# Optimization experiments

Measured on AMD Instinct MI355X. Metric: run time of the kernel, lower is better.

The kernel has to match this reference:

```python
import jax, jax.numpy as jnp
import numpy as np

# alpha clamp limits: balance=False -> [exp(-1/5), exp(-1/25)]
ALPHA_MIN = float(np.exp(-1.0 / 5.0))
ALPHA_MAX = float(np.exp(-1.0 / 25.0))
T_CROP = 100


def setup_inputs() -> dict:
    key = jax.random.key(0)
    k1, k2, k3 = jax.random.split(key, 3)
    B, T, D, H = 128, 1000, 1024, 256
    x = jax.random.normal(k1, (B, T, D), dtype=jnp.float32)
    bound = float(np.sqrt(1.0 / D))
    W = jax.random.uniform(k2, (H, D), minval=-bound, maxval=bound, dtype=jnp.float32)
    alpha = jax.random.uniform(k3, (H,), minval=ALPHA_MIN, maxval=ALPHA_MAX, dtype=jnp.float32)
    return {"x": x, "W": W, "alpha": alpha}


def reference(x, W, alpha):
    # x: [B, T, D], W: [H, D], alpha: [H]
    a = jnp.clip(alpha, ALPHA_MIN, ALPHA_MAX)
    Wx = jnp.einsum('btd,hd->bth', x, W)  # [B, T, H]
    T = Wx.shape[1]
    mask = (jnp.arange(T) >= T_CROP).astype(Wx.dtype)  # [T]
    Wx_t = jnp.moveaxis(Wx, 1, 0)  # [T, B, H]

    def step(carry, inp):
        ut, out = carry
        wx, m = inp
        ut = a * ut + (1.0 - a) * wx
        out = out + m * jax.nn.softmax(ut, axis=-1)
        return (ut, out), None

    B, H = Wx.shape[0], Wx.shape[2]
    init = (jnp.zeros((B, H), Wx.dtype), jnp.zeros((B, H), Wx.dtype))
    (_, out), _ = jax.lax.scan(step, init, (Wx_t, mask))
    return out  # [B, H]
```

## Files before the change

kernel.cpp:

```cpp
#include <hip/hip_runtime.h>
#include <hip/hip_bf16.h>

#define B_    128
#define T_    1000
#define D_    1024
#define H_    256
#define TCROP 100
#define CHUNK 20
#define NCH   50
#define CSKIP 5

typedef __attribute__((ext_vector_type(8))) short bfrag8;
typedef __attribute__((ext_vector_type(4))) float f32x4;
typedef unsigned long long ull;

__device__ __forceinline__ unsigned short f2bf(float f) {
    union { float f; unsigned int u; } v; v.f = f;
    unsigned int u = v.u;
    u += 0x7FFFu + ((u >> 16) & 1u);
    return (unsigned short)(u >> 16);
}
__device__ __forceinline__ float bf2f(unsigned short u) {
    union { unsigned int u; float f; } v; v.u = ((unsigned int)u) << 16;
    return v.f;
}
__device__ __forceinline__ bfrag8 cvt8(float4 f0, float4 f1) {
    bfrag8 v;
    v[0] = (short)f2bf(f0.x); v[1] = (short)f2bf(f0.y);
    v[2] = (short)f2bf(f0.z); v[3] = (short)f2bf(f0.w);
    v[4] = (short)f2bf(f1.x); v[5] = (short)f2bf(f1.y);
    v[6] = (short)f2bf(f1.z); v[7] = (short)f2bf(f1.w);
    return v;
}

__global__ __launch_bounds__(256) void wconv_kernel(
        const float* __restrict__ W, unsigned short* __restrict__ Wbf) {
    const int i = (blockIdx.x * 256 + threadIdx.x) * 8;
    float4 f0 = *(const float4*)(W + i);
    float4 f1 = *(const float4*)(W + i + 4);
    *(bfrag8*)(Wbf + i) = cvt8(f0, f1);
}

__global__ __launch_bounds__(512) void gemm_kernel(
        const float* __restrict__ x, const unsigned short* __restrict__ Wbf,
        unsigned short* __restrict__ Wx) {
    __shared__ unsigned short As[2][128 * 64];
    __shared__ unsigned short Bs[2][256 * 64];

    const int tid  = threadIdx.x;
    const int lane = tid & 63;
    const int wave = tid >> 6;
    const int wr   = wave >> 2;
    const int wc   = wave & 3;
    const int m0   = blockIdx.x * 128;

    f32x4 acc[4][4];
#pragma unroll
    for (int m = 0; m < 4; ++m)
#pragma unroll
        for (int n = 0; n < 4; ++n) acc[m][n] = (f32x4){0.f, 0.f, 0.f, 0.f};

    const int rr  = lane & 15;
    const int kh  = lane >> 4;
    const int ra0 = tid >> 3;
    const int ja  = tid & 7;
    const int sa  = (ja ^ (ra0 & 7)) * 8;
    const float* ap0 = x + (size_t)(m0 + ra0) * D_ + ja * 8;
    const float* ap1 = ap0 + (size_t)64 * D_;

#pragma unroll
    for (int q = 0; q < 4; ++q) {
        const int li = q * 512 + tid;
        const int r = li >> 3, j = li & 7;
        const int jj = j ^ (r & 7);
        __builtin_amdgcn_global_load_lds(
            (const __attribute__((address_space(1))) void*)(Wbf + (size_t)r * D_ + jj * 8),
            (__attribute__((address_space(3))) void*)&Bs[0][li * 8], 16, 0, 0);
    }
    {
        float4 f00 = *(const float4*)ap0;
        float4 f01 = *(const float4*)(ap0 + 4);
        float4 f10 = *(const float4*)ap1;
        float4 f11 = *(const float4*)(ap1 + 4);
        *(bfrag8*)&As[0][ra0 * 64 + sa]        = cvt8(f00, f01);
        *(bfrag8*)&As[0][(ra0 + 64) * 64 + sa] = cvt8(f10, f11);
    }
    asm volatile("s_waitcnt vmcnt(0) lgkmcnt(0)" ::: "memory");
    __builtin_amdgcn_sched_barrier(0);
    __builtin_amdgcn_s_barrier();

    for (int it = 0; it < 16; ++it) {
        const int cur = it & 1, nxt = cur ^ 1;
        float4 f00, f01, f10, f11;
        if (it < 15) {
            const int ktn = (it + 1) * 64;
            f00 = *(const float4*)(ap0 + ktn);
            f01 = *(const float4*)(ap0 + ktn + 4);
            f10 = *(const float4*)(ap1 + ktn);
            f11 = *(const float4*)(ap1 + ktn + 4);
#pragma unroll
            for (int q = 0; q < 4; ++q) {
                const int li = q * 512 + tid;
                const int r = li >> 3, j = li & 7;
                const int jj = j ^ (r & 7);
                __builtin_amdgcn_global_load_lds(
                    (const __attribute__((address_space(1))) void*)
                        (Wbf + (size_t)r * D_ + ktn + jj * 8),
                    (__attribute__((address_space(3))) void*)&Bs[nxt][li * 8], 16, 0, 0);
            }
        }
        __builtin_amdgcn_sched_barrier(0);
#pragma unroll
        for (int kk = 0; kk < 2; ++kk) {
            const int c16 = kk * 4 + kh;
            bfrag8 af[4], bfr[4];
#pragma unroll
            for (int m = 0; m < 4; ++m) {
                const int row = wr * 64 + m * 16 + rr;
                af[m] = *(const bfrag8*)&As[cur][row * 64 + ((c16 ^ (row & 7)) * 8)];
            }
#pragma unroll
            for (int n = 0; n < 4; ++n) {
                const int row = wc * 64 + n * 16 + rr;
                bfr[n] = *(const bfrag8*)&Bs[cur][row * 64 + ((c16 ^ (row & 7)) * 8)];
            }
#pragma unroll
            for (int m = 0; m < 4; ++m)
#pragma unroll
                for (int n = 0; n < 4; ++n)
                    acc[m][n] = __builtin_amdgcn_mfma_f32_16x16x32_bf16(
                        af[m], bfr[n], acc[m][n], 0, 0, 0);
        }
        if (it < 15) {
            *(bfrag8*)&As[nxt][ra0 * 64 + sa]        = cvt8(f00, f01);
            *(bfrag8*)&As[nxt][(ra0 + 64) * 64 + sa] = cvt8(f10, f11);
        }
        asm volatile("s_waitcnt vmcnt(0) lgkmcnt(0)" ::: "memory");
        __builtin_amdgcn_sched_barrier(0);
        __builtin_amdgcn_s_barrier();
    }

    const int cl = lane & 15, rg = lane >> 4;
#pragma unroll
    for (int m = 0; m < 4; ++m)
#pragma unroll
        for (int n = 0; n < 4; ++n)
#pragma unroll
            for (int j = 0; j < 4; ++j) {
                const int row = m0 + wr * 64 + m * 16 + rg * 4 + j;
                const int col = wc * 64 + n * 16 + cl;
                Wx[(size_t)row * H_ + col] = f2bf(acc[m][n][j]);
            }
}

__global__ __launch_bounds__(64) void scanA_kernel(
        const unsigned short* __restrict__ Wx, const float* __restrict__ alpha,
        float* __restrict__ F) {
    const int c = blockIdx.x, b = blockIdx.y;
    const int lane = threadIdx.x;
    const int h = lane * 4;

    const float AMIN = 0.81873075307798182f, AMAX = 0.96078943915232320f;
    float4 al = *(const float4*)(alpha + h);
    float a[4]  = {fminf(fmaxf(al.x, AMIN), AMAX), fminf(fmaxf(al.y, AMIN), AMAX),
                   fminf(fmaxf(al.z, AMIN), AMAX), fminf(fmaxf(al.w, AMIN), AMAX)};
    float om[4] = {1.f - a[0], 1.f - a[1], 1.f - a[2], 1.f - a[3]};

    float ut[4] = {0.f, 0.f, 0.f, 0.f};
    const unsigned short* base = Wx + ((size_t)b * T_ + c * CHUNK) * H_ + h;
#pragma unroll 4
    for (int t = 0; t < CHUNK; ++t) {
        ull wv = *(const ull*)(base + (size_t)t * H_);
        ut[0] = a[0] * ut[0] + om[0] * bf2f((unsigned short)wv);
        ut[1] = a[1] * ut[1] + om[1] * bf2f((unsigned short)(wv >> 16));
        ut[2] = a[2] * ut[2] + om[2] * bf2f((unsigned short)(wv >> 32));
        ut[3] = a[3] * ut[3] + om[3] * bf2f((unsigned short)(wv >> 48));
    }
    float4 o; o.x = ut[0]; o.y = ut[1]; o.z = ut[2]; o.w = ut[3];
    *(float4*)(F + ((size_t)b * NCH + c) * H_ + h) = o;
}

__global__ __launch_bounds__(256) void scanB_kernel(
        const float* __restrict__ F, const float* __restrict__ alpha,
        float* __restrict__ S) {
    const int b = blockIdx.x, h = threadIdx.x;
    const float AMIN = 0.81873075307798182f, AMAX = 0.96078943915232320f;
    const float a = fminf(fmaxf(alpha[h], AMIN), AMAX);
    const float aL = powf(a, (float)CHUNK);
    float s = 0.f;
    for (int c = 0; c < NCH; ++c) {
        S[((size_t)b * NCH + c) * H_ + h] = s;
        s = aL * s + F[((size_t)b * NCH + c) * H_ + h];
    }
}

__global__ __launch_bounds__(64) void scanC_kernel(
        const unsigned short* __restrict__ Wx, const float* __restrict__ alpha,
        const float* __restrict__ S, float* __restrict__ P) {
    const int c = blockIdx.x + CSKIP;
    const int b = blockIdx.y;
    const int lane = threadIdx.x;
    const int h = lane * 4;

    const float AMIN = 0.81873075307798182f, AMAX = 0.96078943915232320f;
    float4 al = *(const float4*)(alpha + h);
    float a[4]  = {fminf(fmaxf(al.x, AMIN), AMAX), fminf(fmaxf(al.y, AMIN), AMAX),
                   fminf(fmaxf(al.z, AMIN), AMAX), fminf(fmaxf(al.w, AMIN), AMAX)};
    float om[4] = {1.f - a[0], 1.f - a[1], 1.f - a[2], 1.f - a[3]};

    float4 s0 = *(const float4*)(S + ((size_t)b * NCH + c) * H_ + h);
    float ut[4]   = {s0.x, s0.y, s0.z, s0.w};
    float acc4[4] = {0.f, 0.f, 0.f, 0.f};

    const unsigned short* base = Wx + ((size_t)b * T_ + c * CHUNK) * H_ + h;
#pragma unroll
    for (int tb = 0; tb < CHUNK; tb += 4) {
        float e[4][4], sl[4];
#pragma unroll
        for (int q = 0; q < 4; ++q) {
            ull wv = *(const ull*)(base + (size_t)(tb + q) * H_);
            ut[0] = a[0] * ut[0] + om[0] * bf2f((unsigned short)wv);
            ut[1] = a[1] * ut[1] + om[1] * bf2f((unsigned short)(wv >> 16));
            ut[2] = a[2] * ut[2] + om[2] * bf2f((unsigned short)(wv >> 32));
            ut[3] = a[3] * ut[3] + om[3] * bf2f((unsigned short)(wv >> 48));
            e[q][0] = __expf(ut[0]);
            e[q][1] = __expf(ut[1]);
            e[q][2] = __expf(ut[2]);
            e[q][3] = __expf(ut[3]);
            sl[q] = (e[q][0] + e[q][1]) + (e[q][2] + e[q][3]);
        }
#pragma unroll
        for (int d = 1; d < 64; d <<= 1) {
            sl[0] += __shfl_xor(sl[0], d);
            sl[1] += __shfl_xor(sl[1], d);
            sl[2] += __shfl_xor(sl[2], d);
            sl[3] += __shfl_xor(sl[3], d);
        }
#pragma unroll
        for (int q = 0; q < 4; ++q) {
            const float rcp = 1.0f / sl[q];
            acc4[0] += e[q][0] * rcp;
            acc4[1] += e[q][1] * rcp;
            acc4[2] += e[q][2] * rcp;
            acc4[3] += e[q][3] * rcp;
        }
    }
    float4 o; o.x = acc4[0]; o.y = acc4[1]; o.z = acc4[2]; o.w = acc4[3];
    *(float4*)(P + ((size_t)b * NCH + c) * H_ + h) = o;
}

__global__ __launch_bounds__(256) void scanD_kernel(
        const float* __restrict__ P, float* __restrict__ out) {
    const int b = blockIdx.x, h = threadIdx.x;
    float s = 0.f;
    for (int c = CSKIP; c < NCH; ++c) s += P[((size_t)b * NCH + c) * H_ + h];
    out[(size_t)b * H_ + h] = s;
}

extern "C" void kernel_launch(void* const* d_in, const int* in_sizes, int n_in,
                              void* d_out, int out_size, void* d_ws, size_t ws_size,
                              hipStream_t stream) {
    const float* x     = (const float*)d_in[0];
    const float* W     = (const float*)d_in[1];
    const float* alpha = (const float*)d_in[2];
    float* out = (float*)d_out;

    char* ws = (char*)d_ws;
    unsigned short* Wbf = (unsigned short*)ws;
    unsigned short* Wx  = (unsigned short*)(ws + ((size_t)1 << 20));
    float* F = (float*)(ws + ((size_t)70 << 20));
    float* S = (float*)(ws + ((size_t)80 << 20));
    float* P = (float*)(ws + ((size_t)90 << 20));

    wconv_kernel<<<128, 256, 0, stream>>>(W, Wbf);
    gemm_kernel<<<(B_ * T_) / 128, 512, 0, stream>>>(x, Wbf, Wx);
    scanA_kernel<<<dim3(NCH, B_), 64, 0, stream>>>(Wx, alpha, F);
    scanB_kernel<<<B_, H_, 0, stream>>>(F, alpha, S);
    scanC_kernel<<<dim3(NCH - CSKIP, B_), 64, 0, stream>>>(Wx, alpha, S, P);
    scanD_kernel<<<B_, H_, 0, stream>>>(P, out);
}
```

Before: 209.6 us.

## Fuse chunk-local EMA scan into GEMM epilogue and fold carry into softmax pass

The GEMM now tiles per (batch, 125-step chunk) and, after the MFMA loop, stages the bf16 tile in shared memory so 256 threads can run the local EMA recurrence. They write the local EMA state (only for t>=100) plus the chunk-end carry. The separate scanA and scanB kernels are removed, and scanC rebuilds the carry prefix from the chunk carries and adds the decayed carry to the stored local state before the softmax. This removes one pass over Wx and two launches, but the GEMM loses double buffering (single LDS buffer with syncthreads). It also wastes 3 of 128 rows per tile and adds a serial 125-step scan to each block, with only 1024 blocks.

```diff
diff --git a/kernel.cpp b/kernel.cpp
--- a/kernel.cpp
+++ b/kernel.cpp
@@ -6,9 +6,9 @@
 #define D_    1024
 #define H_    256
 #define TCROP 100
-#define CHUNK 20
-#define NCH   50
-#define CSKIP 5
+#define CHK   125
+#define NC    8
+#define NOUT  900
 
 typedef __attribute__((ext_vector_type(8))) short bfrag8;
 typedef __attribute__((ext_vector_type(4))) float f32x4;
@@ -41,18 +41,22 @@
     *(bfrag8*)(Wbf + i) = cvt8(f0, f1);
 }
 
-__global__ __launch_bounds__(512) void gemm_kernel(
+__global__ __launch_bounds__(512) void gemm_ema_kernel(
         const float* __restrict__ x, const unsigned short* __restrict__ Wbf,
-        unsigned short* __restrict__ Wx) {
-    __shared__ unsigned short As[2][128 * 64];
-    __shared__ unsigned short Bs[2][256 * 64];
+        const float* __restrict__ alpha,
+        unsigned short* __restrict__ utl, float* __restrict__ F) {
+    __shared__ unsigned short smem[128 * 256];
+    unsigned short* As = smem;
+    unsigned short* Bs = smem + 128 * 64;
 
     const int tid  = threadIdx.x;
     const int lane = tid & 63;
     const int wave = tid >> 6;
     const int wr   = wave >> 2;
     const int wc   = wave & 3;
-    const int m0   = blockIdx.x * 128;
+    const int c    = blockIdx.x;
+    const int b    = blockIdx.y;
+    const int m0   = b * T_ + c * CHK;
 
     f32x4 acc[4][4];
 #pragma unroll
@@ -65,51 +69,37 @@
     const int ra0 = tid >> 3;
     const int ja  = tid & 7;
     const int sa  = (ja ^ (ra0 & 7)) * 8;
+    const int rA1 = (ra0 + 64 < CHK) ? (ra0 + 64) : (CHK - 1);
     const float* ap0 = x + (size_t)(m0 + ra0) * D_ + ja * 8;
-    const float* ap1 = ap0 + (size_t)64 * D_;
-
-#pragma unroll
-    for (int q = 0; q < 4; ++q) {
-        const int li = q * 512 + tid;
-        const int r = li >> 3, j = li & 7;
-        const int jj = j ^ (r & 7);
-        __builtin_amdgcn_global_load_lds(
-            (const __attribute__((address_space(1))) void*)(Wbf + (size_t)r * D_ + jj * 8),
-            (__attribute__((address_space(3))) void*)&Bs[0][li * 8], 16, 0, 0);
-    }
-    {
-        float4 f00 = *(const float4*)ap0;
-        float4 f01 = *(const float4*)(ap0 + 4);
-        float4 f10 = *(const float4*)ap1;
-        float4 f11 = *(const float4*)(ap1 + 4);
-        *(bfrag8*)&As[0][ra0 * 64 + sa]        = cvt8(f00, f01);
-        *(bfrag8*)&As[0][(ra0 + 64) * 64 + sa] = cvt8(f10, f11);
-    }
-    asm volatile("s_waitcnt vmcnt(0) lgkmcnt(0)" ::: "memory");
-    __builtin_amdgcn_sched_barrier(0);
-    __builtin_amdgcn_s_barrier();
+    const float* ap1 = x + (size_t)(m0 + rA1) * D_ + ja * 8;
+
+    float4 p00 = *(const float4*)ap0;
+    float4 p01 = *(const float4*)(ap0 + 4);
+    float4 p10 = *(const float4*)ap1;
+    float4 p11 = *(const float4*)(ap1 + 4);
 
     for (int it = 0; it < 16; ++it) {
-        const int cur = it & 1, nxt = cur ^ 1;
-        float4 f00, f01, f10, f11;
+        const int kt = it * 64;
+#pragma unroll
+        for (int q = 0; q < 4; ++q) {
+            const int li = q * 512 + tid;
+            const int r = li >> 3, j = li & 7;
+            const int jj = j ^ (r & 7);
+            __builtin_amdgcn_global_load_lds(
+                (const __attribute__((address_space(1))) void*)
+                    (Wbf + (size_t)r * D_ + kt + jj * 8),
+                (__attribute__((address_space(3))) void*)&Bs[li * 8], 16, 0, 0);
+        }
+        *(bfrag8*)&As[ra0 * 64 + sa]        = cvt8(p00, p01);
+        *(bfrag8*)&As[(ra0 + 64) * 64 + sa] = cvt8(p10, p11);
+        __syncthreads();
         if (it < 15) {
-            const int ktn = (it + 1) * 64;
-            f00 = *(const float4*)(ap0 + ktn);
-            f01 = *(const float4*)(ap0 + ktn + 4);
-            f10 = *(const float4*)(ap1 + ktn);
-            f11 = *(const float4*)(ap1 + ktn + 4);
-#pragma unroll
-            for (int q = 0; q < 4; ++q) {
-                const int li = q * 512 + tid;
-                const int r = li >> 3, j = li & 7;
-                const int jj = j ^ (r & 7);
-                __builtin_amdgcn_global_load_lds(
-                    (const __attribute__((address_space(1))) void*)
-                        (Wbf + (size_t)r * D_ + ktn + jj * 8),
-                    (__attribute__((address_space(3))) void*)&Bs[nxt][li * 8], 16, 0, 0);
-            }
-        }
-        __builtin_amdgcn_sched_barrier(0);
+            const int ktn = kt + 64;
+            p00 = *(const float4*)(ap0 + ktn);
+            p01 = *(const float4*)(ap0 + ktn + 4);
+            p10 = *(const float4*)(ap1 + ktn);
+            p11 = *(const float4*)(ap1 + ktn + 4);
+        }
 #pragma unroll
         for (int kk = 0; kk < 2; ++kk) {
             const int c16 = kk * 4 + kh;
@@ -117,12 +107,12 @@
 #pragma unroll
             for (int m = 0; m < 4; ++m) {
                 const int row = wr * 64 + m * 16 + rr;
-                af[m] = *(const bfrag8*)&As[cur][row * 64 + ((c16 ^ (row & 7)) * 8)];
+                af[m] = *(const bfrag8*)&As[row * 64 + ((c16 ^ (row & 7)) * 8)];
             }
 #pragma unroll
             for (int n = 0; n < 4; ++n) {
                 const int row = wc * 64 + n * 16 + rr;
-                bfr[n] = *(const bfrag8*)&Bs[cur][row * 64 + ((c16 ^ (row & 7)) * 8)];
+                bfr[n] = *(const bfrag8*)&Bs[row * 64 + ((c16 ^ (row & 7)) * 8)];
             }
 #pragma unroll
             for (int m = 0; m < 4; ++m)
@@ -131,13 +121,7 @@
                     acc[m][n] = __builtin_amdgcn_mfma_f32_16x16x32_bf16(
                         af[m], bfr[n], acc[m][n], 0, 0, 0);
         }
-        if (it < 15) {
-            *(bfrag8*)&As[nxt][ra0 * 64 + sa]        = cvt8(f00, f01);
-            *(bfrag8*)&As[nxt][(ra0 + 64) * 64 + sa] = cvt8(f10, f11);
-        }
-        asm volatile("s_waitcnt vmcnt(0) lgkmcnt(0)" ::: "memory");
-        __builtin_amdgcn_sched_barrier(0);
-        __builtin_amdgcn_s_barrier();
+        __syncthreads();
     }
 
     const int cl = lane & 15, rg = lane >> 4;
@@ -147,97 +131,88 @@
         for (int n = 0; n < 4; ++n)
 #pragma unroll
             for (int j = 0; j < 4; ++j) {
-                const int row = m0 + wr * 64 + m * 16 + rg * 4 + j;
-                const int col = wc * 64 + n * 16 + cl;
-                Wx[(size_t)row * H_ + col] = f2bf(acc[m][n][j]);
+                const int row = wr * 64 + m * 16 + rg * 4 + j;
+                const int col = (wc * 64 + n * 16 + cl + rg * 16) & 255;
+                smem[row * 256 + col] = f2bf(acc[m][n][j]);
             }
-}
-
-__global__ __launch_bounds__(64) void scanA_kernel(
-        const unsigned short* __restrict__ Wx, const float* __restrict__ alpha,
-        float* __restrict__ F) {
+    __syncthreads();
+
+    if (tid < H_) {
+        const int h = tid;
+        const float AMIN = 0.81873075307798182f, AMAX = 0.96078943915232320f;
+        const float a  = fminf(fmaxf(alpha[h], AMIN), AMAX);
+        const float om = 1.0f - a;
+        float ut = 0.f;
+        const int t0 = c * CHK;
+        for (int r = 0; r < CHK; ++r) {
+            const int col = (h + ((r >> 2) & 3) * 16) & 255;
+            ut = a * ut + om * bf2f(smem[r * 256 + col]);
+            const int t = t0 + r;
+            if (t >= TCROP)
+                utl[((size_t)b * NOUT + (t - TCROP)) * H_ + h] = f2bf(ut);
+        }
+        F[((size_t)b * NC + c) * H_ + h] = ut;
+    }
+}
+
+__global__ __launch_bounds__(64) void scanC_kernel(
+        const unsigned short* __restrict__ utl, const float* __restrict__ alpha,
+        const float* __restrict__ F, float* __restrict__ P) {
     const int c = blockIdx.x, b = blockIdx.y;
     const int lane = threadIdx.x;
-    const int h = lane * 4;
+    const int h4 = lane * 4;
 
     const float AMIN = 0.81873075307798182f, AMAX = 0.96078943915232320f;
-    float4 al = *(const float4*)(alpha + h);
-    float a[4]  = {fminf(fmaxf(al.x, AMIN), AMAX), fminf(fmaxf(al.y, AMIN), AMAX),
-                   fminf(fmaxf(al.z, AMIN), AMAX), fminf(fmaxf(al.w, AMIN), AMAX)};
-    float om[4] = {1.f - a[0], 1.f - a[1], 1.f - a[2], 1.f - a[3]};
-
-    float ut[4] = {0.f, 0.f, 0.f, 0.f};
-    const unsigned short* base = Wx + ((size_t)b * T_ + c * CHUNK) * H_ + h;
-#pragma unroll 4
-    for (int t = 0; t < CHUNK; ++t) {
-        ull wv = *(const ull*)(base + (size_t)t * H_);
-        ut[0] = a[0] * ut[0] + om[0] * bf2f((unsigned short)wv);
-        ut[1] = a[1] * ut[1] + om[1] * bf2f((unsigned short)(wv >> 16));
-        ut[2] = a[2] * ut[2] + om[2] * bf2f((unsigned short)(wv >> 32));
-        ut[3] = a[3] * ut[3] + om[3] * bf2f((unsigned short)(wv >> 48));
-    }
-    float4 o; o.x = ut[0]; o.y = ut[1]; o.z = ut[2]; o.w = ut[3];
-    *(float4*)(F + ((size_t)b * NCH + c) * H_ + h) = o;
-}
-
-__global__ __launch_bounds__(256) void scanB_kernel(
-        const float* __restrict__ F, const float* __restrict__ alpha,
-        float* __restrict__ S) {
-    const int b = blockIdx.x, h = threadIdx.x;
-    const float AMIN = 0.81873075307798182f, AMAX = 0.96078943915232320f;
-    const float a = fminf(fmaxf(alpha[h], AMIN), AMAX);
-    const float aL = powf(a, (float)CHUNK);
-    float s = 0.f;
-    for (int c = 0; c < NCH; ++c) {
-        S[((size_t)b * NCH + c) * H_ + h] = s;
-        s = aL * s + F[((size_t)b * NCH + c) * H_ + h];
-    }
-}
-
-__global__ __launch_bounds__(64) void scanC_kernel(
-        const unsigned short* __restrict__ Wx, const float* __restrict__ alpha,
-        const float* __restrict__ S, float* __restrict__ P) {
-    const int c = blockIdx.x + CSKIP;
-    const int b = blockIdx.y;
-    const int lane = threadIdx.x;
-    const int h = lane * 4;
-
-    const float AMIN = 0.81873075307798182f, AMAX = 0.96078943915232320f;
-    float4 al = *(const float4*)(alpha + h);
-    float a[4]  = {fminf(fmaxf(al.x, AMIN), AMAX), fminf(fmaxf(al.y, AMIN), AMAX),
-                   fminf(fmaxf(al.z, AMIN), AMAX), fminf(fmaxf(al.w, AMIN), AMAX)};
-    float om[4] = {1.f - a[0], 1.f - a[1], 1.f - a[2], 1.f - a[3]};
-
-    float4 s0 = *(const float4*)(S + ((size_t)b * NCH + c) * H_ + h);
-    float ut[4]   = {s0.x, s0.y, s0.z, s0.w};
+    float4 al = *(const float4*)(alpha + h4);
+    float a[4] = {fminf(fmaxf(al.x, AMIN), AMAX), fminf(fmaxf(al.y, AMIN), AMAX),
+                  fminf(fmaxf(al.z, AMIN), AMAX), fminf(fmaxf(al.w, AMIN), AMAX)};
+
+    float S[4] = {0.f, 0.f, 0.f, 0.f};
+    if (c > 0) {
+        float aL[4] = {__powf(a[0], (float)CHK), __powf(a[1], (float)CHK),
+                       __powf(a[2], (float)CHK), __powf(a[3], (float)CHK)};
+        for (int j = 0; j < c; ++j) {
+            float4 f = *(const float4*)(F + ((size_t)b * NC + j) * H_ + h4);
+            S[0] = aL[0] * S[0] + f.x;
+            S[1] = aL[1] * S[1] + f.y;
+            S[2] = aL[2] * S[2] + f.z;
+            S[3] = aL[3] * S[3] + f.w;
+        }
+    }
+
+    const int nt = (c == 0) ? (CHK - TCROP) : CHK;
+    const size_t ti0 = (size_t)b * NOUT + (c == 0 ? 0 : c * CHK - TCROP);
+    const unsigned short* base = utl + ti0 * H_ + h4;
+
+    float d[4]    = {1.f, 1.f, 1.f, 1.f};
     float acc4[4] = {0.f, 0.f, 0.f, 0.f};
 
-    const unsigned short* base = Wx + ((size_t)b * T_ + c * CHUNK) * H_ + h;
-#pragma unroll
-    for (int tb = 0; tb < CHUNK; tb += 4) {
-        float e[4][4], sl[4];
-#pragma unroll
-        for (int q = 0; q < 4; ++q) {
-            ull wv = *(const ull*)(base + (size_t)(tb + q) * H_);
-            ut[0] = a[0] * ut[0] + om[0] * bf2f((unsigned short)wv);
-            ut[1] = a[1] * ut[1] + om[1] * bf2f((unsigned short)(wv >> 16));
-            ut[2] = a[2] * ut[2] + om[2] * bf2f((unsigned short)(wv >> 32));
-            ut[3] = a[3] * ut[3] + om[3] * bf2f((unsigned short)(wv >> 48));
-            e[q][0] = __expf(ut[0]);
-            e[q][1] = __expf(ut[1]);
-            e[q][2] = __expf(ut[2]);
-            e[q][3] = __expf(ut[3]);
+    for (int bb = 0; bb < nt; bb += 5) {
+        float e[5][4], sl[5];
+#pragma unroll
+        for (int q = 0; q < 5; ++q) {
+            ull wv = *(const ull*)(base + (size_t)(bb + q) * H_);
+            d[0] *= a[0]; d[1] *= a[1]; d[2] *= a[2]; d[3] *= a[3];
+            float u0 = bf2f((unsigned short)wv)         + d[0] * S[0];
+            float u1 = bf2f((unsigned short)(wv >> 16)) + d[1] * S[1];
+            float u2 = bf2f((unsigned short)(wv >> 32)) + d[2] * S[2];
+            float u3 = bf2f((unsigned short)(wv >> 48)) + d[3] * S[3];
+            e[q][0] = __expf(u0);
+            e[q][1] = __expf(u1);
+            e[q][2] = __expf(u2);
+            e[q][3] = __expf(u3);
             sl[q] = (e[q][0] + e[q][1]) + (e[q][2] + e[q][3]);
         }
 #pragma unroll
-        for (int d = 1; d < 64; d <<= 1) {
-            sl[0] += __shfl_xor(sl[0], d);
-            sl[1] += __shfl_xor(sl[1], d);
-            sl[2] += __shfl_xor(sl[2], d);
-            sl[3] += __shfl_xor(sl[3], d);
-        }
-#pragma unroll
-        for (int q = 0; q < 4; ++q) {
+        for (int dd = 1; dd < 64; dd <<= 1) {
+            sl[0] += __shfl_xor(sl[0], dd);
+            sl[1] += __shfl_xor(sl[1], dd);
+            sl[2] += __shfl_xor(sl[2], dd);
+            sl[3] += __shfl_xor(sl[3], dd);
+            sl[4] += __shfl_xor(sl[4], dd);
+        }
+#pragma unroll
+        for (int q = 0; q < 5; ++q) {
             const float rcp = 1.0f / sl[q];
             acc4[0] += e[q][0] * rcp;
             acc4[1] += e[q][1] * rcp;
@@ -246,14 +221,15 @@
         }
     }
     float4 o; o.x = acc4[0]; o.y = acc4[1]; o.z = acc4[2]; o.w = acc4[3];
-    *(float4*)(P + ((size_t)b * NCH + c) * H_ + h) = o;
+    *(float4*)(P + ((size_t)b * NC + c) * H_ + h4) = o;
 }
 
 __global__ __launch_bounds__(256) void scanD_kernel(
         const float* __restrict__ P, float* __restrict__ out) {
     const int b = blockIdx.x, h = threadIdx.x;
     float s = 0.f;
-    for (int c = CSKIP; c < NCH; ++c) s += P[((size_t)b * NCH + c) * H_ + h];
+#pragma unroll
+    for (int c = 0; c < NC; ++c) s += P[((size_t)b * NC + c) * H_ + h];
     out[(size_t)b * H_ + h] = s;
 }
 
@@ -267,15 +243,12 @@
 
     char* ws = (char*)d_ws;
     unsigned short* Wbf = (unsigned short*)ws;
-    unsigned short* Wx  = (unsigned short*)(ws + ((size_t)1 << 20));
-    float* F = (float*)(ws + ((size_t)70 << 20));
-    float* S = (float*)(ws + ((size_t)80 << 20));
-    float* P = (float*)(ws + ((size_t)90 << 20));
+    unsigned short* utl = (unsigned short*)(ws + ((size_t)1 << 20));
+    float* F = (float*)(ws + ((size_t)64 << 20));
+    float* P = (float*)(ws + ((size_t)66 << 20));
 
     wconv_kernel<<<128, 256, 0, stream>>>(W, Wbf);
-    gemm_kernel<<<(B_ * T_) / 128, 512, 0, stream>>>(x, Wbf, Wx);
-    scanA_kernel<<<dim3(NCH, B_), 64, 0, stream>>>(Wx, alpha, F);
-    scanB_kernel<<<B_, H_, 0, stream>>>(F, alpha, S);
-    scanC_kernel<<<dim3(NCH - CSKIP, B_), 64, 0, stream>>>(Wx, alpha, S, P);
-    scanD_kernel<<<B_, H_, 0, stream>>>(P, out);
-}
+    gemm_ema_kernel<<<dim3(NC, B_), 512, 0, stream>>>(x, Wbf, alpha, utl, F);
+    scanC_kernel<<<dim3(NC, B_), 64, 0, stream>>>(utl, alpha, F, P);
+    scanD_kernel<<<B_, 256, 0, stream>>>(P, out);
+}
```

New measurement: 205.3 us. 2.0% less time.
